# Kernel tuning notes

Hardware: AMD Instinct MI355X
Metric: run time of the kernel (lower is better)

## Reference

```python
import jax, jax.numpy as jnp
import numpy as np

POWER = 2.0
EPS = jnp.float32(np.finfo(np.float32).eps)


def setup_inputs() -> dict:
    key = jax.random.key(0)
    k1, k2, k3 = jax.random.split(key, 3)
    B, P, S = 2, 131072, 512
    station_coords = jax.random.uniform(k1, (B, S, 2), dtype=jnp.float32)
    station_values = jax.random.normal(k2, (B, S), dtype=jnp.float32)
    grid_points = jax.random.uniform(k3, (B, P, 2), dtype=jnp.float32)
    return {
        "station_coords": station_coords,
        "station_values": station_values,
        "grid_points": grid_points,
    }


def reference(station_coords, station_values, grid_points):
    # grid_points: (B, P, 2); station_coords: (B, S, 2)
    diff = grid_points[:, :, None, :] - station_coords[:, None, :, :]  # (B, P, S, 2)
    distances = jnp.sqrt(jnp.sum(diff * diff, axis=-1))                # (B, P, S)
    distances = jnp.where(distances == 0, EPS, distances)
    weights = 1.0 / distances ** POWER                                  # (B, P, S)
    weights_sum = jnp.sum(weights, axis=-1)                             # (B, P)
    interpolated = jnp.sum(weights * station_values[:, None, :], axis=-1) / weights_sum
    return interpolated  # (B, P)
```

## Files before the change

kernel.cpp:

```cpp
#include <hip/hip_runtime.h>
#include <hip/hip_bf16.h>


#define BLOCK 256
#define S_MAX 512
#define GPT 2

__global__ __launch_bounds__(BLOCK) void idw_kernel(
    const float* __restrict__ station_coords,
    const float* __restrict__ station_values,
    const float* __restrict__ grid_points,
    float* __restrict__ out,
    int P, int S) {

    __shared__ float st[S_MAX * 3];

    const int b = blockIdx.y;
    const float2* __restrict__ sc2 = (const float2*)(station_coords) + (size_t)b * S;
    const float*  __restrict__ svb = station_values + (size_t)b * S;

    for (int i = threadIdx.x; i < S; i += BLOCK) {
        const float2 c = sc2[i];
        st[3 * i + 0] = c.x;
        st[3 * i + 1] = c.y;
        st[3 * i + 2] = svb[i];
    }
    __syncthreads();

    const int tid = blockIdx.x * BLOCK + threadIdx.x;
    const float4 g01 = ((const float4*)grid_points)[(size_t)b * (P / 2) + tid];
    const float gx0 = g01.x, gy0 = g01.y, gx1 = g01.z, gy1 = g01.w;

    constexpr float EPS  = 1.1920928955078125e-07f;
    constexpr float EPS2 = EPS * EPS;

    float wsum0 = 0.0f, vsum0 = 0.0f;
    float wsum1 = 0.0f, vsum1 = 0.0f;

    const float4* __restrict__ st4 = (const float4*)st;

    auto quad = [&](float gx, float gy, float& ws, float& vs,
                    const float4& f0, const float4& f1, const float4& f2) {
        const float dxa = gx - f0.x, dya = gy - f0.y;
        const float a = fmaf(dxa, dxa, fmaf(dya, dya, EPS2));
        const float dxb = gx - f0.w, dyb = gy - f1.x;
        const float bq = fmaf(dxb, dxb, fmaf(dyb, dyb, EPS2));
        const float dxc = gx - f1.z, dyc = gy - f1.w;
        const float c = fmaf(dxc, dxc, fmaf(dyc, dyc, EPS2));
        const float dxd = gx - f2.y, dyd = gy - f2.z;
        const float d = fmaf(dxd, dxd, fmaf(dyd, dyd, EPS2));
        const float pab = a * bq, pcd = c * d;
        const float sab = a + bq, scd = c + d;
        const float nab = fmaf(f1.y, a, f0.z * bq);
        const float ncd = fmaf(f2.w, c, f2.x * d);
        const float r = __builtin_amdgcn_rcpf(pab * pcd);
        ws = fmaf(fmaf(sab, pcd, scd * pab), r, ws);
        vs = fmaf(fmaf(nab, pcd, ncd * pab), r, vs);
    };

    float4 c0 = st4[0], c1 = st4[1], c2 = st4[2];
#pragma unroll 4
    for (int k = 0; k < S_MAX / 4 - 1; ++k) {
        const float4 n0 = st4[3 * k + 3];
        const float4 n1 = st4[3 * k + 4];
        const float4 n2 = st4[3 * k + 5];
        quad(gx0, gy0, wsum0, vsum0, c0, c1, c2);
        quad(gx1, gy1, wsum1, vsum1, c0, c1, c2);
        c0 = n0; c1 = n1; c2 = n2;
    }
    quad(gx0, gy0, wsum0, vsum0, c0, c1, c2);
    quad(gx1, gy1, wsum1, vsum1, c0, c1, c2);

    const float r0 = vsum0 / wsum0;
    const float r1 = vsum1 / wsum1;
    ((float2*)out)[(size_t)b * (P / 2) + tid] = make_float2(r0, r1);
}

extern "C" void kernel_launch(void* const* d_in, const int* in_sizes, int n_in,
                              void* d_out, int out_size, void* d_ws, size_t ws_size,
                              hipStream_t stream) {
    const float* station_coords = (const float*)d_in[0];
    const float* station_values = (const float*)d_in[1];
    const float* grid_points    = (const float*)d_in[2];
    float* out = (float*)d_out;

    const int B = 2;
    const int S = in_sizes[1] / B;
    const int P = out_size / B;

    dim3 grid(P / (BLOCK * GPT), B);
    dim3 block(BLOCK);
    idw_kernel<<<grid, block, 0, stream>>>(station_coords, station_values,
                                           grid_points, out, P, S);
}
```

Baseline: 79.67 us.

## Read station data via constant address space scalar loads instead of LDS staging

Removes the shared-memory staging of station coordinates and values, together with the block barrier. Station data is instead read directly from global memory through address_space(4) pointers, so the compiler can emit uniform scalar loads (s_load) into SGPRs. This is meant to cut LDS traffic and the barrier. In exchange the loop depends on scalar cache latency and SGPR pressure, and the station count is hardcoded to 512.

```diff
diff --git a/kernel.cpp b/kernel.cpp
--- a/kernel.cpp
+++ b/kernel.cpp
@@ -1,10 +1,11 @@
 #include <hip/hip_runtime.h>
-#include <hip/hip_bf16.h>
 
 
 #define BLOCK 256
-#define S_MAX 512
 #define GPT 2
+
+typedef float v4f __attribute__((ext_vector_type(4)));
+typedef const __attribute__((address_space(4))) v4f k_v4f;
 
 __global__ __launch_bounds__(BLOCK) void idw_kernel(
     const float* __restrict__ station_coords,
@@ -13,19 +14,10 @@
     float* __restrict__ out,
     int P, int S) {
 
-    __shared__ float st[S_MAX * 3];
+    const int b = blockIdx.y;
 
-    const int b = blockIdx.y;
-    const float2* __restrict__ sc2 = (const float2*)(station_coords) + (size_t)b * S;
-    const float*  __restrict__ svb = station_values + (size_t)b * S;
-
-    for (int i = threadIdx.x; i < S; i += BLOCK) {
-        const float2 c = sc2[i];
-        st[3 * i + 0] = c.x;
-        st[3 * i + 1] = c.y;
-        st[3 * i + 2] = svb[i];
-    }
-    __syncthreads();
+    k_v4f* sc4 = (k_v4f*)(station_coords + (size_t)b * S * 2);
+    k_v4f* sv4 = (k_v4f*)(station_values + (size_t)b * S);
 
     const int tid = blockIdx.x * BLOCK + threadIdx.x;
     const float4 g01 = ((const float4*)grid_points)[(size_t)b * (P / 2) + tid];
@@ -37,39 +29,33 @@
     float wsum0 = 0.0f, vsum0 = 0.0f;
     float wsum1 = 0.0f, vsum1 = 0.0f;
 
-    const float4* __restrict__ st4 = (const float4*)st;
-
     auto quad = [&](float gx, float gy, float& ws, float& vs,
-                    const float4& f0, const float4& f1, const float4& f2) {
-        const float dxa = gx - f0.x, dya = gy - f0.y;
+                    v4f cAB, v4f cCD, v4f vv) {
+        const float dxa = gx - cAB.x, dya = gy - cAB.y;
         const float a = fmaf(dxa, dxa, fmaf(dya, dya, EPS2));
-        const float dxb = gx - f0.w, dyb = gy - f1.x;
+        const float dxb = gx - cAB.z, dyb = gy - cAB.w;
         const float bq = fmaf(dxb, dxb, fmaf(dyb, dyb, EPS2));
-        const float dxc = gx - f1.z, dyc = gy - f1.w;
+        const float dxc = gx - cCD.x, dyc = gy - cCD.y;
         const float c = fmaf(dxc, dxc, fmaf(dyc, dyc, EPS2));
-        const float dxd = gx - f2.y, dyd = gy - f2.z;
+        const float dxd = gx - cCD.z, dyd = gy - cCD.w;
         const float d = fmaf(dxd, dxd, fmaf(dyd, dyd, EPS2));
         const float pab = a * bq, pcd = c * d;
         const float sab = a + bq, scd = c + d;
-        const float nab = fmaf(f1.y, a, f0.z * bq);
-        const float ncd = fmaf(f2.w, c, f2.x * d);
+        const float nab = fmaf(vv.y, a, vv.x * bq);
+        const float ncd = fmaf(vv.w, c, vv.z * d);
         const float r = __builtin_amdgcn_rcpf(pab * pcd);
         ws = fmaf(fmaf(sab, pcd, scd * pab), r, ws);
         vs = fmaf(fmaf(nab, pcd, ncd * pab), r, vs);
     };
 
-    float4 c0 = st4[0], c1 = st4[1], c2 = st4[2];
 #pragma unroll 4
-    for (int k = 0; k < S_MAX / 4 - 1; ++k) {
-        const float4 n0 = st4[3 * k + 3];
-        const float4 n1 = st4[3 * k + 4];
-        const float4 n2 = st4[3 * k + 5];
-        quad(gx0, gy0, wsum0, vsum0, c0, c1, c2);
-        quad(gx1, gy1, wsum1, vsum1, c0, c1, c2);
-        c0 = n0; c1 = n1; c2 = n2;
+    for (int k = 0; k < 512 / 4; ++k) {
+        const v4f cAB = sc4[2 * k + 0];
+        const v4f cCD = sc4[2 * k + 1];
+        const v4f vv  = sv4[k];
+        quad(gx0, gy0, wsum0, vsum0, cAB, cCD, vv);
+        quad(gx1, gy1, wsum1, vsum1, cAB, cCD, vv);
     }
-    quad(gx0, gy0, wsum0, vsum0, c0, c1, c2);
-    quad(gx1, gy1, wsum1, vsum1, c0, c1, c2);
 
     const float r0 = vsum0 / wsum0;
     const float r1 = vsum1 / wsum1;
```

New measurement: 79.91 us. No clear change (+0.3%).

## Split stations across wavefront teams with 4 points per thread and LDS reduction

Applied to the files above, without the earlier changes.

Each block now handles 256 points, and its four wavefronts each process a quarter of the stations. Every lane handles 4 grid points, so each LDS station load is reused across more points. The partial weight and value sums go through shared memory and are combined before the division. This doubles the block count and cuts LDS traffic per computation, at the cost of an extra barrier, more registers, and the removal of the software-prefetch pipelining.

```diff
diff --git a/kernel.cpp b/kernel.cpp
--- a/kernel.cpp
+++ b/kernel.cpp
@@ -1,10 +1,11 @@
 #include <hip/hip_runtime.h>
-#include <hip/hip_bf16.h>
 
 
 #define BLOCK 256
 #define S_MAX 512
-#define GPT 2
+#define TEAMS 4
+#define S_PER_TEAM (S_MAX / TEAMS)
+#define CHUNKS (S_PER_TEAM / 4)
 
 __global__ __launch_bounds__(BLOCK) void idw_kernel(
     const float* __restrict__ station_coords,
@@ -13,7 +14,8 @@
     float* __restrict__ out,
     int P, int S) {
 
-    __shared__ float st[S_MAX * 3];
+    __shared__ float  st[S_MAX * 3];
+    __shared__ float2 part[TEAMS][BLOCK];
 
     const int b = blockIdx.y;
     const float2* __restrict__ sc2 = (const float2*)(station_coords) + (size_t)b * S;
@@ -27,17 +29,21 @@
     }
     __syncthreads();
 
-    const int tid = blockIdx.x * BLOCK + threadIdx.x;
-    const float4 g01 = ((const float4*)grid_points)[(size_t)b * (P / 2) + tid];
-    const float gx0 = g01.x, gy0 = g01.y, gx1 = g01.z, gy1 = g01.w;
+    const int team = threadIdx.x >> 6;
+    const int lane = threadIdx.x & 63;
+
+    const int pbase = blockIdx.x * BLOCK + 4 * lane;
+    const float4* __restrict__ gp4 = (const float4*)(grid_points + (size_t)b * P * 2);
+    const float4 gA = gp4[pbase / 2 + 0];
+    const float4 gB = gp4[pbase / 2 + 1];
+    const float gx0 = gA.x, gy0 = gA.y, gx1 = gA.z, gy1 = gA.w;
+    const float gx2 = gB.x, gy2 = gB.y, gx3 = gB.z, gy3 = gB.w;
 
     constexpr float EPS  = 1.1920928955078125e-07f;
     constexpr float EPS2 = EPS * EPS;
 
-    float wsum0 = 0.0f, vsum0 = 0.0f;
-    float wsum1 = 0.0f, vsum1 = 0.0f;
-
-    const float4* __restrict__ st4 = (const float4*)st;
+    float ws0 = 0.f, vs0 = 0.f, ws1 = 0.f, vs1 = 0.f;
+    float ws2 = 0.f, vs2 = 0.f, ws3 = 0.f, vs3 = 0.f;
 
     auto quad = [&](float gx, float gy, float& ws, float& vs,
                     const float4& f0, const float4& f1, const float4& f2) {
@@ -58,22 +64,30 @@
         vs = fmaf(fmaf(nab, pcd, ncd * pab), r, vs);
     };
 
-    float4 c0 = st4[0], c1 = st4[1], c2 = st4[2];
+    const float4* __restrict__ stt = (const float4*)(st + 3 * S_PER_TEAM * team);
+
 #pragma unroll 4
-    for (int k = 0; k < S_MAX / 4 - 1; ++k) {
-        const float4 n0 = st4[3 * k + 3];
-        const float4 n1 = st4[3 * k + 4];
-        const float4 n2 = st4[3 * k + 5];
-        quad(gx0, gy0, wsum0, vsum0, c0, c1, c2);
-        quad(gx1, gy1, wsum1, vsum1, c0, c1, c2);
-        c0 = n0; c1 = n1; c2 = n2;
+    for (int k = 0; k < CHUNKS; ++k) {
+        const float4 f0 = stt[3 * k + 0];
+        const float4 f1 = stt[3 * k + 1];
+        const float4 f2 = stt[3 * k + 2];
+        quad(gx0, gy0, ws0, vs0, f0, f1, f2);
+        quad(gx1, gy1, ws1, vs1, f0, f1, f2);
+        quad(gx2, gy2, ws2, vs2, f0, f1, f2);
+        quad(gx3, gy3, ws3, vs3, f0, f1, f2);
     }
-    quad(gx0, gy0, wsum0, vsum0, c0, c1, c2);
-    quad(gx1, gy1, wsum1, vsum1, c0, c1, c2);
 
-    const float r0 = vsum0 / wsum0;
-    const float r1 = vsum1 / wsum1;
-    ((float2*)out)[(size_t)b * (P / 2) + tid] = make_float2(r0, r1);
+    part[team][4 * lane + 0] = make_float2(ws0, vs0);
+    part[team][4 * lane + 1] = make_float2(ws1, vs1);
+    part[team][4 * lane + 2] = make_float2(ws2, vs2);
+    part[team][4 * lane + 3] = make_float2(ws3, vs3);
+    __syncthreads();
+
+    const int t = threadIdx.x;
+    const float2 a0 = part[0][t], a1 = part[1][t], a2 = part[2][t], a3 = part[3][t];
+    const float W = (a0.x + a1.x) + (a2.x + a3.x);
+    const float V = (a0.y + a1.y) + (a2.y + a3.y);
+    out[(size_t)b * P + blockIdx.x * BLOCK + t] = V / W;
 }
 
 extern "C" void kernel_launch(void* const* d_in, const int* in_sizes, int n_in,
@@ -88,7 +102,7 @@
     const int S = in_sizes[1] / B;
     const int P = out_size / B;
 
-    dim3 grid(P / (BLOCK * GPT), B);
+    dim3 grid(P / BLOCK, B);
     dim3 block(BLOCK);
     idw_kernel<<<grid, block, 0, stream>>>(station_coords, station_values,
                                            grid_points, out, P, S);
```

After: 82.66 us. 1.04x slower.
